# Performance work log

Measured on AMD Instinct MI355X. Metric: run time of the kernel, lower is better.

The kernel has to match this reference:

```python
import jax, jax.numpy as jnp
import numpy as np

OUT_SIZE = (7, 7, 7)
SPATIAL_SCALE = 1.0
SAMPLING_RATIO = 2
ALIGNED = True


def setup_inputs() -> dict:
    key = jax.random.key(0)
    kf, kc1, kc2 = jax.random.split(key, 3)
    B, C, D, H, W = 2, 128, 16, 64, 64
    N = 64
    features = jax.random.normal(kf, (B, C, D, H, W), dtype=jnp.float32)
    # Build valid boxes (z1,y1,x1,z2,y2,x2) inside the feature volume.
    dims = jnp.array([D, H, W], dtype=jnp.float32)
    lo = jax.random.uniform(kc1, (B, N, 3)) * dims * 0.6
    ext = 2.0 + jax.random.uniform(kc2, (B, N, 3)) * dims * 0.35
    hi = jnp.minimum(lo + ext, dims - 1.0)
    rois = jnp.concatenate([lo, hi], axis=-1).astype(jnp.float32)  # [B,N,6]
    return {"features": features, "rois": rois}


def _trilinear_sample(feat, z, y, x):
    # feat: [C,D,H,W]; z,y,x: [N,Pd,Ph,Pw] pixel coords (align_corners=False,
    # zero padding: out-of-bounds corners contribute 0).
    C, D, H, W = feat.shape
    z0f, y0f, x0f = jnp.floor(z), jnp.floor(y), jnp.floor(x)
    lz, ly, lx = z - z0f, y - y0f, x - x0f
    z0 = z0f.astype(jnp.int32)
    y0 = y0f.astype(jnp.int32)
    x0 = x0f.astype(jnp.int32)
    feat_flat = feat.reshape(C, -1)  # [C, D*H*W]

    def corner(zi, yi, xi, w):
        valid = ((zi >= 0) & (zi < D) & (yi >= 0) & (yi < H) & (xi >= 0) & (xi < W))
        idx = (jnp.clip(zi, 0, D - 1) * H + jnp.clip(yi, 0, H - 1)) * W + jnp.clip(xi, 0, W - 1)
        vals = jnp.take(feat_flat, idx.reshape(-1), axis=1).reshape((C,) + idx.shape)
        return vals * (w * valid.astype(w.dtype))[None]

    out = corner(z0, y0, x0, (1 - lz) * (1 - ly) * (1 - lx))
    out = out + corner(z0, y0, x0 + 1, (1 - lz) * (1 - ly) * lx)
    out = out + corner(z0, y0 + 1, x0, (1 - lz) * ly * (1 - lx))
    out = out + corner(z0, y0 + 1, x0 + 1, (1 - lz) * ly * lx)
    out = out + corner(z0 + 1, y0, x0, lz * (1 - ly) * (1 - lx))
    out = out + corner(z0 + 1, y0, x0 + 1, lz * (1 - ly) * lx)
    out = out + corner(z0 + 1, y0 + 1, x0, lz * ly * (1 - lx))
    out = out + corner(z0 + 1, y0 + 1, x0 + 1, lz * ly * lx)
    return out  # [C,N,Pd,Ph,Pw]


def _roi_align_3d(features, rois):
    B, C, D, H, W = features.shape
    od, oh, ow = OUT_SIZE
    s = SAMPLING_RATIO if SAMPLING_RATIO > 0 else 1
    dt = features.dtype
    d_step = (jnp.arange(od * s, dtype=dt) + 0.5) / s
    h_step = (jnp.arange(oh * s, dtype=dt) + 0.5) / s
    w_step = (jnp.arange(ow * s, dtype=dt) + 0.5) / s

    def per_batch(feat, roi):  # feat [C,D,H,W], roi [N,6]
        roi = roi * SPATIAL_SCALE
        if ALIGNED:
            roi = roi - 0.5
        z1, y1, x1, z2, y2, x2 = (roi[:, i] for i in range(6))
        bd = jnp.maximum(z2 - z1, 1e-6) / od
        bh = jnp.maximum(y2 - y1, 1e-6) / oh
        bw = jnp.maximum(x2 - x1, 1e-6) / ow
        zg = z1[:, None] + d_step[None, :] * bd[:, None]  # [N, od*s]
        yg = y1[:, None] + h_step[None, :] * bh[:, None]  # [N, oh*s]
        xg = x1[:, None] + w_step[None, :] * bw[:, None]  # [N, ow*s]
        z, y, x = jnp.broadcast_arrays(zg[:, :, None, None], yg[:, None, :, None], xg[:, None, None, :])
        sam = _trilinear_sample(feat, z, y, x)  # [C,N,od*s,oh*s,ow*s]
        N = roi.shape[0]
        sam = sam.reshape(C, N, od, s, oh, s, ow, s).mean(axis=(3, 5, 7))
        return sam.transpose(1, 0, 2, 3, 4)  # [N,C,od,oh,ow]

    return jax.vmap(per_batch)(features, rois)  # [B,N,C,od,oh,ow]


def reference(features, rois):
    return _roi_align_3d(features, rois)
```

## Files before the change

kernel.cpp:

```cpp
#include <hip/hip_runtime.h>

constexpr int Bc = 2, Nc = 64, Cc = 128, Dc = 16, Hc = 64, Wc = 64;
constexpr int OD = 7, OH = 7, OW = 7;
constexpr int CELLS = OD * OH * OW;
constexpr int DHW = Dc * Hc * Wc, HW = Hc * Wc;
constexpr int MAXZ = 10, MAXY = 25, MAXX = 25;
constexpr int SUBSZ = MAXZ * MAXY * (MAXX + 1);
constexpr int BLOB = 176;
constexpr int TZP = 0, WZP = 28, TYP = 56, WYB = 84, WXB = 112, TXO = 140;
constexpr int TBLN = 154;

typedef _Float16 h2f __attribute__((ext_vector_type(2)));

__device__ inline unsigned pk_f16(float a, float b) {
    return __builtin_bit_cast(unsigned, __builtin_amdgcn_cvt_pkrtz(a, b));
}
__device__ inline h2f uh(unsigned u) { return __builtin_bit_cast(h2f, u); }

__global__ __launch_bounds__(128) void roi_pre(
    const float* __restrict__ rois, unsigned* __restrict__ ws)
{
    int r = threadIdx.x;
    if (r >= Bc * Nc) return;
    const float* rp = rois + r * 6;
    float r1a[3] = {rp[0] - 0.5f, rp[1] - 0.5f, rp[2] - 0.5f};
    float r2a[3] = {rp[3] - 0.5f, rp[4] - 0.5f, rp[5] - 0.5f};
    const int dims[3] = {Dc, Hc, Wc};
    const int maxn[3] = {MAXZ, MAXY, MAXX};
    float bs[3]; int lo[3], ncnt[3];
    #pragma unroll
    for (int a = 0; a < 3; ++a) {
        bs[a] = fmaxf(r2a[a] - r1a[a], 1e-6f) * (1.0f / 7.0f);
        float smin = r1a[a] + 0.25f * bs[a];
        float smax = r1a[a] + 6.75f * bs[a];
        int l = max(0, (int)floorf(smin));
        int h = min(dims[a] - 1, (int)floorf(smax) + 1);
        lo[a] = l;
        ncnt[a] = min(h - l + 1, maxn[a]);
    }
    int zn = ncnt[0], yn = ncnt[1], xn = ncnt[2];
    int xnp = xn | 1;
    int rows = zn * yn;
    int total = rows * xnp;
    int zstride = yn * xnp;
    int gz = lo[0] * HW + lo[1] * Wc + lo[2];
    unsigned m32x = 0xFFFFFFFFu / (unsigned)xnp + 1u;
    unsigned m32y = 0xFFFFFFFFu / (unsigned)yn + 1u;

    unsigned* blob = ws + r * BLOB;
    blob[0] = (unsigned)total; blob[1] = (unsigned)xnp; blob[2] = (unsigned)xn;
    blob[3] = (unsigned)yn;    blob[4] = (unsigned)gz;  blob[5] = m32x;
    blob[6] = m32y;            blob[7] = (unsigned)zn;  blob[8] = (unsigned)zstride;
    blob[9] = 0;
    unsigned* tb = blob + 10;
    for (int m = 0; m < 14; ++m) {
        #pragma unroll
        for (int a = 0; a < 3; ++a) {
            float v = r1a[a] + ((float)m + 0.5f) * 0.5f * bs[a];
            float f = floorf(v);
            float l = v - f;
            int i0 = (int)f;
            int d  = dims[a];
            float w0 = (i0 >= 0 && i0 < d) ? 1.0f - l : 0.0f;
            float w1 = (i0 + 1 < d) ? l : 0.0f;
            if (a == 0) {
                int c0 = min(max(i0 - lo[0], 0), zn - 1);
                int c1 = min(max(i0 + 1 - lo[0], 0), zn - 1);
                tb[TZP + 2 * m]     = (unsigned)c0;
                tb[TZP + 2 * m + 1] = (unsigned)c1;
                ((float*)tb)[WZP + 2 * m]     = w0;
                ((float*)tb)[WZP + 2 * m + 1] = w1;
            } else if (a == 1) {
                int c0 = min(max(i0 - lo[1], 0), yn - 1);
                int c1 = min(max(i0 + 1 - lo[1], 0), yn - 1);
                tb[TYP + 2 * m]     = (unsigned)(c0 * xnp);
                tb[TYP + 2 * m + 1] = (unsigned)(c1 * xnp);
                tb[WYB + 2 * m]     = pk_f16(w0, w0);
                tb[WYB + 2 * m + 1] = pk_f16(w1, w1);
            } else {
                int c0 = min(max(i0 - lo[2], -1), xn - 1);
                tb[TXO + m] = (unsigned)c0;
                tb[WXB + 2 * m]     = pk_f16(w0, w0);
                tb[WXB + 2 * m + 1] = pk_f16(w1, w1);
            }
        }
    }
}

__global__ __launch_bounds__(384) void roialign3d_v12(
    const float* __restrict__ feat, const unsigned* __restrict__ ws,
    float* __restrict__ out)
{
    __shared__ __align__(16) unsigned sub[SUBSZ + 2];
    __shared__ __align__(16) unsigned tbl[TBLN];

    const int blk = blockIdx.x;
    const int cp  = blk & 63;
    const int n   = (blk >> 6) & 63;
    const int b   = blk >> 12;
    const int tid = threadIdx.x;

    const unsigned* blob = ws + (unsigned)(b * Nc + n) * BLOB;
    const int total   = (int)blob[0];
    const int xnp     = (int)blob[1];
    const int xn      = (int)blob[2];
    const int yn      = (int)blob[3];
    const int gz      = (int)blob[4];
    const unsigned m32x = blob[5];
    const unsigned m32y = blob[6];
    const int zn      = (int)blob[7];
    const int zstride = (int)blob[8];

    if (tid < TBLN) tbl[tid] = blob[10 + tid];
    if (tid == 352) sub[0] = 0;
    if (tid == 353) sub[1 + total] = 0;

    const int c0ch = cp * 2;
    const float* fb = feat + ((size_t)b * Cc + c0ch) * DHW;
    for (int p = tid; p < total; p += 384) {
        int row = (int)__umulhi((unsigned)p, m32x);
        int x   = p - row * xnp;
        int xs  = min(x, xn - 1);
        int z   = (int)__umulhi((unsigned)row, m32y);
        int y   = row - z * yn;
        int g   = gz + (z << 12) + (y << 6) + xs;
        sub[1 + p] = pk_f16(fb[g], fb[g + DHW]);
    }
    __syncthreads();

    if (tid < CELLS) {
        int i   = tid / 49;
        int rem = tid - i * 49;
        int j   = rem / 7;
        int k   = rem - j * 7;
        int4   tzr = *(const int4*)&tbl[TZP + 4 * i];
        float4 wzv = *(const float4*)&tbl[WZP + 4 * i];
        int4   ty  = *(const int4*)&tbl[TYP + 4 * j];
        uint4  wyb = *(const uint4*)&tbl[WYB + 4 * j];
        uint4  wxb = *(const uint4*)&tbl[WXB + 4 * k];
        int xo0 = (int)tbl[TXO + 2 * k], xo1 = (int)tbl[TXO + 2 * k + 1];

        const unsigned* G = sub + 1;
        h2f wx00 = uh(wxb.x), wx01 = uh(wxb.y);
        h2f wx10 = uh(wxb.z), wx11 = uh(wxb.w);
        const h2f wys[4] = {uh(wyb.x), uh(wyb.y), uh(wyb.z), uh(wyb.w)};

        int c0z = tzr.x;
        int p1 = tzr.y - c0z, p2 = tzr.z - c0z, p3 = tzr.w - c0z;
        float cz0 = wzv.x + (p1 == 0 ? wzv.y : 0.0f)
                  + (p2 == 0 ? wzv.z : 0.0f) + (p3 == 0 ? wzv.w : 0.0f);
        float cz1 = (p1 == 1 ? wzv.y : 0.0f)
                  + (p2 == 1 ? wzv.z : 0.0f) + (p3 == 1 ? wzv.w : 0.0f);
        float cz2 = (p3 == 2 ? wzv.w : 0.0f);
        int zb0 = c0z * zstride;
        int zb1 = min(c0z + 1, zn - 1) * zstride;
        int zb2 = min(c0z + 2, zn - 1) * zstride;

        const int   zbs[3] = {zb0, zb1, zb2};
        const float czs[3] = {cz0, cz1, cz2};
        const int   yo[4]  = {ty.x, ty.y, ty.z, ty.w};

        float a0 = 0.0f, a1 = 0.0f;
        #pragma unroll
        for (int d = 0; d < 3; ++d) {
            int zb = zbs[d];
            h2f s = {(_Float16)0, (_Float16)0};
            #pragma unroll
            for (int yi = 0; yi < 4; ++yi) {
                int base = zb + yo[yi];
                h2f A0 = uh(G[base + xo0]), A1 = uh(G[base + xo0 + 1]);
                h2f B0 = uh(G[base + xo1]), B1 = uh(G[base + xo1 + 1]);
                h2f xr = A0 * wx00 + A1 * wx01 + B0 * wx10 + B1 * wx11;
                s = s + wys[yi] * xr;
            }
            a0 = fmaf(czs[d], (float)s.x, a0);
            a1 = fmaf(czs[d], (float)s.y, a1);
        }
        size_t obase = ((size_t)(b * Nc + n) * Cc + c0ch) * CELLS;
        out[obase + tid]         = a0 * 0.125f;
        out[obase + CELLS + tid] = a1 * 0.125f;
    }
}

extern "C" void kernel_launch(void* const* d_in, const int* in_sizes, int n_in,
                              void* d_out, int out_size, void* d_ws, size_t ws_size,
                              hipStream_t stream) {
    const float* feat = (const float*)d_in[0];
    const float* rois = (const float*)d_in[1];
    float* out = (float*)d_out;
    unsigned* ws = (unsigned*)d_ws;
    hipLaunchKernelGGL(roi_pre, dim3(1), dim3(128), 0, stream, rois, ws);
    hipLaunchKernelGGL(roialign3d_v12, dim3(Bc * Nc * (Cc / 2)), dim3(384), 0,
                       stream, feat, (const unsigned*)ws, out);
}
```

Before: 44.09 us.

## Load feature pairs as float2 with even-aligned x and read tables from global

Aligns each ROI's x-window start to an even index and pads rows to a bucketed even stride. The staging loop can then load two adjacent x values per channel with float2 loads and store them as a uint2 to LDS, halving the loop trip count and the index arithmetic. The shared table copy is removed: per-cell weights are read straight from the global workspace before the barrier, and the z-weight setup is also moved ahead of the barrier so it overlaps with staging. In exchange, the padded row layout uses more LDS per block, and the right-edge clamp logic is more complex.

```diff
diff --git a/kernel.cpp b/kernel.cpp
--- a/kernel.cpp
+++ b/kernel.cpp
@@ -4,11 +4,10 @@
 constexpr int OD = 7, OH = 7, OW = 7;
 constexpr int CELLS = OD * OH * OW;
 constexpr int DHW = Dc * Hc * Wc, HW = Hc * Wc;
-constexpr int MAXZ = 10, MAXY = 25, MAXX = 25;
-constexpr int SUBSZ = MAXZ * MAXY * (MAXX + 1);
+constexpr int MAXZ = 10, MAXY = 25;
+constexpr int SUBSZ = MAXZ * MAXY * 26;
 constexpr int BLOB = 176;
 constexpr int TZP = 0, WZP = 28, TYP = 56, WYB = 84, WXB = 112, TXO = 140;
-constexpr int TBLN = 154;
 
 typedef _Float16 h2f __attribute__((ext_vector_type(2)));
 
@@ -26,7 +25,7 @@
     float r1a[3] = {rp[0] - 0.5f, rp[1] - 0.5f, rp[2] - 0.5f};
     float r2a[3] = {rp[3] - 0.5f, rp[4] - 0.5f, rp[5] - 0.5f};
     const int dims[3] = {Dc, Hc, Wc};
-    const int maxn[3] = {MAXZ, MAXY, MAXX};
+    const int maxn[3] = {MAXZ, MAXY, 25};
     float bs[3]; int lo[3], ncnt[3];
     #pragma unroll
     for (int a = 0; a < 3; ++a) {
@@ -38,21 +37,27 @@
         lo[a] = l;
         ncnt[a] = min(h - l + 1, maxn[a]);
     }
+    {
+        int l = lo[2] & ~1;
+        ncnt[2] = min(ncnt[2] + (lo[2] - l), 26);
+        lo[2] = l;
+    }
     int zn = ncnt[0], yn = ncnt[1], xn = ncnt[2];
-    int xnp = xn | 1;
+    int s  = (xn <= 14) ? 14 : (xn <= 18) ? 18 : (xn <= 22) ? 22 : 26;
+    int hp = s >> 1;
     int rows = zn * yn;
-    int total = rows * xnp;
-    int zstride = yn * xnp;
+    int zstride = yn * s;
     int gz = lo[0] * HW + lo[1] * Wc + lo[2];
-    unsigned m32x = 0xFFFFFFFFu / (unsigned)xnp + 1u;
+    unsigned m32p = 0xFFFFFFFFu / (unsigned)hp + 1u;
     unsigned m32y = 0xFFFFFFFFu / (unsigned)yn + 1u;
 
     unsigned* blob = ws + r * BLOB;
-    blob[0] = (unsigned)total; blob[1] = (unsigned)xnp; blob[2] = (unsigned)xn;
-    blob[3] = (unsigned)yn;    blob[4] = (unsigned)gz;  blob[5] = m32x;
-    blob[6] = m32y;            blob[7] = (unsigned)zn;  blob[8] = (unsigned)zstride;
-    blob[9] = 0;
-    unsigned* tb = blob + 10;
+    blob[0] = (unsigned)(rows * hp);
+    blob[1] = (unsigned)hp;  blob[2] = (unsigned)xn;  blob[3] = (unsigned)yn;
+    blob[4] = (unsigned)gz;  blob[5] = m32p;  blob[6] = m32y;
+    blob[7] = (unsigned)zn;  blob[8] = (unsigned)zstride;
+    blob[9] = (unsigned)s;
+    unsigned* tb = blob + 12;
     for (int m = 0; m < 14; ++m) {
         #pragma unroll
         for (int a = 0; a < 3; ++a) {
@@ -73,8 +78,8 @@
             } else if (a == 1) {
                 int c0 = min(max(i0 - lo[1], 0), yn - 1);
                 int c1 = min(max(i0 + 1 - lo[1], 0), yn - 1);
-                tb[TYP + 2 * m]     = (unsigned)(c0 * xnp);
-                tb[TYP + 2 * m + 1] = (unsigned)(c1 * xnp);
+                tb[TYP + 2 * m]     = (unsigned)(c0 * s);
+                tb[TYP + 2 * m + 1] = (unsigned)(c1 * s);
                 tb[WYB + 2 * m]     = pk_f16(w0, w0);
                 tb[WYB + 2 * m + 1] = pk_f16(w1, w1);
             } else {
@@ -87,12 +92,11 @@
     }
 }
 
-__global__ __launch_bounds__(384) void roialign3d_v12(
+__global__ __launch_bounds__(384) void roialign3d_v13(
     const float* __restrict__ feat, const unsigned* __restrict__ ws,
     float* __restrict__ out)
 {
     __shared__ __align__(16) unsigned sub[SUBSZ + 2];
-    __shared__ __align__(16) unsigned tbl[TBLN];
 
     const int blk = blockIdx.x;
     const int cp  = blk & 63;
@@ -101,80 +105,97 @@
     const int tid = threadIdx.x;
 
     const unsigned* blob = ws + (unsigned)(b * Nc + n) * BLOB;
-    const int total   = (int)blob[0];
-    const int xnp     = (int)blob[1];
+    const int totalp  = (int)blob[0];
+    const int hp      = (int)blob[1];
     const int xn      = (int)blob[2];
     const int yn      = (int)blob[3];
     const int gz      = (int)blob[4];
-    const unsigned m32x = blob[5];
+    const unsigned m32p = blob[5];
     const unsigned m32y = blob[6];
     const int zn      = (int)blob[7];
     const int zstride = (int)blob[8];
-
-    if (tid < TBLN) tbl[tid] = blob[10 + tid];
-    if (tid == 352) sub[0] = 0;
-    if (tid == 353) sub[1 + total] = 0;
-
-    const int c0ch = cp * 2;
-    const float* fb = feat + ((size_t)b * Cc + c0ch) * DHW;
-    for (int p = tid; p < total; p += 384) {
-        int row = (int)__umulhi((unsigned)p, m32x);
-        int x   = p - row * xnp;
-        int xs  = min(x, xn - 1);
-        int z   = (int)__umulhi((unsigned)row, m32y);
-        int y   = row - z * yn;
-        int g   = gz + (z << 12) + (y << 6) + xs;
-        sub[1 + p] = pk_f16(fb[g], fb[g + DHW]);
-    }
-    __syncthreads();
-
-    if (tid < CELLS) {
+    const unsigned* tb = blob + 12;
+
+    const bool isCell = tid < CELLS;
+    int4 tzr; float4 wzv; int4 ty; uint4 wyb, wxb; int2 xop;
+    if (isCell) {
         int i   = tid / 49;
         int rem = tid - i * 49;
         int j   = rem / 7;
         int k   = rem - j * 7;
-        int4   tzr = *(const int4*)&tbl[TZP + 4 * i];
-        float4 wzv = *(const float4*)&tbl[WZP + 4 * i];
-        int4   ty  = *(const int4*)&tbl[TYP + 4 * j];
-        uint4  wyb = *(const uint4*)&tbl[WYB + 4 * j];
-        uint4  wxb = *(const uint4*)&tbl[WXB + 4 * k];
-        int xo0 = (int)tbl[TXO + 2 * k], xo1 = (int)tbl[TXO + 2 * k + 1];
-
-        const unsigned* G = sub + 1;
+        tzr = *(const int4*)&tb[TZP + 4 * i];
+        wzv = *(const float4*)&tb[WZP + 4 * i];
+        ty  = *(const int4*)&tb[TYP + 4 * j];
+        wyb = *(const uint4*)&tb[WYB + 4 * j];
+        wxb = *(const uint4*)&tb[WXB + 4 * k];
+        xop = *(const int2*)&tb[TXO + 2 * k];
+    }
+    if (tid == 352) sub[0] = 0;
+    if (tid == 353) sub[1] = 0;
+
+    const int c0ch = cp * 2;
+    const float* fb = feat + ((size_t)b * Cc + c0ch) * DHW;
+    for (int p = tid; p < totalp; p += 384) {
+        int row = (int)__umulhi((unsigned)p, m32p);
+        int t   = p - row * hp;
+        int x0  = t << 1;
+        int z   = (int)__umulhi((unsigned)row, m32y);
+        int y   = row - z * yn;
+        int g   = gz + (z << 12) + (y << 6) + x0;
+        unsigned d0, d1;
+        if (x0 + 1 < xn) {
+            float2 va = *(const float2*)(fb + g);
+            float2 vb = *(const float2*)(fb + g + DHW);
+            d0 = pk_f16(va.x, vb.x);
+            d1 = pk_f16(va.y, vb.y);
+        } else {
+            int gc = g - (x0 - (xn - 1));
+            d0 = pk_f16(fb[gc], fb[gc + DHW]);
+            d1 = d0;
+        }
+        *(uint2*)&sub[2 + row * (hp << 1) + x0] = make_uint2(d0, d1);
+    }
+
+    int zb0 = 0, zb1 = 0, zb2 = 0; float cz0 = 0, cz1 = 0, cz2 = 0;
+    if (isCell) {
+        int c0z = tzr.x;
+        int p1 = tzr.y - c0z, p2 = tzr.z - c0z, p3 = tzr.w - c0z;
+        cz0 = wzv.x + (p1 == 0 ? wzv.y : 0.0f)
+            + (p2 == 0 ? wzv.z : 0.0f) + (p3 == 0 ? wzv.w : 0.0f);
+        cz1 = (p1 == 1 ? wzv.y : 0.0f)
+            + (p2 == 1 ? wzv.z : 0.0f) + (p3 == 1 ? wzv.w : 0.0f);
+        cz2 = (p3 == 2 ? wzv.w : 0.0f);
+        zb0 = c0z * zstride;
+        zb1 = min(c0z + 1, zn - 1) * zstride;
+        zb2 = min(c0z + 2, zn - 1) * zstride;
+    }
+    __syncthreads();
+
+    if (isCell) {
+        const unsigned* G = sub + 2;
         h2f wx00 = uh(wxb.x), wx01 = uh(wxb.y);
         h2f wx10 = uh(wxb.z), wx11 = uh(wxb.w);
         const h2f wys[4] = {uh(wyb.x), uh(wyb.y), uh(wyb.z), uh(wyb.w)};
-
-        int c0z = tzr.x;
-        int p1 = tzr.y - c0z, p2 = tzr.z - c0z, p3 = tzr.w - c0z;
-        float cz0 = wzv.x + (p1 == 0 ? wzv.y : 0.0f)
-                  + (p2 == 0 ? wzv.z : 0.0f) + (p3 == 0 ? wzv.w : 0.0f);
-        float cz1 = (p1 == 1 ? wzv.y : 0.0f)
-                  + (p2 == 1 ? wzv.z : 0.0f) + (p3 == 1 ? wzv.w : 0.0f);
-        float cz2 = (p3 == 2 ? wzv.w : 0.0f);
-        int zb0 = c0z * zstride;
-        int zb1 = min(c0z + 1, zn - 1) * zstride;
-        int zb2 = min(c0z + 2, zn - 1) * zstride;
-
         const int   zbs[3] = {zb0, zb1, zb2};
         const float czs[3] = {cz0, cz1, cz2};
         const int   yo[4]  = {ty.x, ty.y, ty.z, ty.w};
+        const int xo0 = xop.x, xo1 = xop.y;
 
         float a0 = 0.0f, a1 = 0.0f;
         #pragma unroll
         for (int d = 0; d < 3; ++d) {
             int zb = zbs[d];
-            h2f s = {(_Float16)0, (_Float16)0};
+            h2f sacc = {(_Float16)0, (_Float16)0};
             #pragma unroll
             for (int yi = 0; yi < 4; ++yi) {
                 int base = zb + yo[yi];
                 h2f A0 = uh(G[base + xo0]), A1 = uh(G[base + xo0 + 1]);
                 h2f B0 = uh(G[base + xo1]), B1 = uh(G[base + xo1 + 1]);
                 h2f xr = A0 * wx00 + A1 * wx01 + B0 * wx10 + B1 * wx11;
-                s = s + wys[yi] * xr;
+                sacc = sacc + wys[yi] * xr;
             }
-            a0 = fmaf(czs[d], (float)s.x, a0);
-            a1 = fmaf(czs[d], (float)s.y, a1);
+            a0 = fmaf(czs[d], (float)sacc.x, a0);
+            a1 = fmaf(czs[d], (float)sacc.y, a1);
         }
         size_t obase = ((size_t)(b * Nc + n) * Cc + c0ch) * CELLS;
         out[obase + tid]         = a0 * 0.125f;
@@ -190,6 +211,6 @@
     float* out = (float*)d_out;
     unsigned* ws = (unsigned*)d_ws;
     hipLaunchKernelGGL(roi_pre, dim3(1), dim3(128), 0, stream, rois, ws);
-    hipLaunchKernelGGL(roialign3d_v12, dim3(Bc * Nc * (Cc / 2)), dim3(384), 0,
+    hipLaunchKernelGGL(roialign3d_v13, dim3(Bc * Nc * (Cc / 2)), dim3(384), 0,
                        stream, feat, (const unsigned*)ws, out);
 }
```

Result: slower. 45.45 us (+3.1%).
